# Kernel tuning notes

Hardware: AMD Instinct MI355X
Metric: run time of the kernel (lower is better)

## Reference

```python
import jax, jax.numpy as jnp
import numpy as np

B, T, C = 4, 2048, 1024
N_HEAD = 16
HEAD_DIM = C // N_HEAD


def setup_inputs() -> dict:
    key = jax.random.key(0)
    k1, k2, k3 = jax.random.split(key, 3)
    x = jax.random.normal(k1, (B, T, C), dtype=jnp.float32)
    # Linear weights stored as (in, out); scaled like typical init
    w_qkv = jax.random.normal(k2, (C, 3 * C), dtype=jnp.float32) * (1.0 / np.sqrt(C))
    w_proj = jax.random.normal(k3, (C, C), dtype=jnp.float32) * (1.0 / np.sqrt(C))
    return {"x": x, "w_qkv": w_qkv, "w_proj": w_proj}


def reference(x, w_qkv, w_proj):
    b, t, c = x.shape
    qkv = x @ w_qkv                      # (B,T,3C)
    q, k, v = jnp.split(qkv, 3, axis=-1)
    # (B,H,T,D)
    def to_heads(a):
        return a.reshape(b, t, N_HEAD, HEAD_DIM).transpose(0, 2, 1, 3)
    q, k, v = to_heads(q), to_heads(k), to_heads(v)
    scale = 1.0 / np.sqrt(HEAD_DIM).astype(np.float32)
    att = jnp.einsum('bhqd,bhkd->bhqk', q, k) * scale   # (B,H,T,T)
    causal = jnp.tril(jnp.ones((t, t), dtype=bool))
    att = jnp.where(causal[None, None, :, :], att, -jnp.inf)
    att = jax.nn.softmax(att, axis=-1)
    # dropout p=0.0 (eval) -> identity
    y = jnp.einsum('bhqk,bhkd->bhqd', att, v)            # (B,H,T,D)
    y = y.transpose(0, 2, 1, 3).reshape(b, t, c)
    return y @ w_proj
```

## Files before the change

kernel.cpp:

```cpp
#include <hip/hip_runtime.h>
#include <hip/hip_bf16.h>
#include <stdint.h>

#define Bsz 4
#define Tsz 2048
#define Csz 1024
#define Hn  16
#define Dh  64
#define BH  (Bsz*Hn)
#define Mrows (Bsz*Tsz)
#define N1  (3*Csz)

typedef short s16x8 __attribute__((ext_vector_type(8)));
typedef short s16x4 __attribute__((ext_vector_type(4)));
typedef float fx4   __attribute__((ext_vector_type(4)));

static __device__ __forceinline__ short f2bf(float x) {
  __hip_bfloat16 h = __float2bfloat16(x);
  return __builtin_bit_cast(short, h);
}

#define GLDS16(g, l) __builtin_amdgcn_global_load_lds( \
    (const __attribute__((address_space(1))) void*)(g), \
    (__attribute__((address_space(3))) void*)(l), 16, 0, 0)

__global__ __launch_bounds__(256) void prep_kernel(
    const float* __restrict__ x,  short* __restrict__ xb,
    const float* __restrict__ wq, short* __restrict__ wqT,
    const float* __restrict__ wp, short* __restrict__ wpT)
{
  const int bid = (int)blockIdx.x;
  if (bid < 1024) {
    const int n4 = Mrows*Csz/4;
    int i = bid * 256 + threadIdx.x;
    const int stride = 1024 * 256;
    for (; i < n4; i += stride) {
      float4 v = ((const float4*)x)[i];
      s16x4 o;
      o.x = f2bf(v.x); o.y = f2bf(v.y); o.z = f2bf(v.z); o.w = f2bf(v.w);
      ((s16x4*)xb)[i] = o;
    }
    return;
  }
  const float* w; short* wt; int K, N, tb;
  if (bid < 1024 + 3072) { w = wq; wt = wqT; K = Csz; N = N1;  tb = bid - 1024; }
  else                   { w = wp; wt = wpT; K = Csz; N = Csz; tb = bid - 4096; }
  const int nbx = N >> 5;
  const int n0 = (tb % nbx) * 32;
  const int k0 = (tb / nbx) * 32;
  __shared__ float tile[32][33];
  int tc = threadIdx.x & 31;
  int tr = threadIdx.x >> 5;
#pragma unroll
  for (int p = 0; p < 4; p++) {
    int r = tr + p*8;
    tile[r][tc] = w[(size_t)(k0 + r) * N + (n0 + tc)];
  }
  __syncthreads();
#pragma unroll
  for (int p = 0; p < 4; p++) {
    int r = tr + p*8;
    wt[(size_t)(n0 + r) * K + (k0 + tc)] = f2bf(tile[tc][r]);
  }
}

static __device__ __forceinline__ s16x8 lds_frag(const short* p, int off) {
  return *(const s16x8*)(p + off);
}

#define WAITV(n) __asm__ __volatile__("s_waitcnt vmcnt(" #n ")" ::: "memory")

__global__ __launch_bounds__(512) void gemm_bt_kernel(
    const short* __restrict__ A, const short* __restrict__ Bt,
    float* __restrict__ Cf,
    short* __restrict__ Qo, short* __restrict__ Ko, short* __restrict__ Vo,
    int Mdim, int Ndim, int Kdim, int mode)
{
  __shared__ __align__(16) short sA[3][128*64];
  __shared__ __align__(16) short sB[3][256*64];
  const int tid  = threadIdx.x;
  const int lane = tid & 63;
  const int lr   = lane & 15;
  const int lq   = lane >> 4;
  const int wv   = tid >> 6;
  const int nb   = Ndim >> 8;
  const int nwg  = (int)gridDim.x;
  const int orig = (int)blockIdx.x;
  const int wgid = (orig & 7) * (nwg >> 3) + (orig >> 3);
  const int bm   = wgid / nb;
  const int bn   = wgid % nb;
  const int m_off = (wv & 1) << 6;
  const int n_off = (wv >> 1) << 6;

  const short* Ab = A  + (size_t)bm * 128 * Kdim;
  const short* Bb = Bt + (size_t)bn * 256 * Kdim;

  const short* gA[2];
  const short* gB[4];
#pragma unroll
  for (int j = 0; j < 2; j++) {
    int c = tid + 512*j, r = c >> 3, o = ((c & 7) ^ (r & 7)) * 8;
    gA[j] = Ab + (size_t)r * Kdim + o;
  }
#pragma unroll
  for (int j = 0; j < 4; j++) {
    int c = tid + 512*j, r = c >> 3, o = ((c & 7) ^ (r & 7)) * 8;
    gB[j] = Bb + (size_t)r * Kdim + o;
  }

  int offA[4][2], offB[4][2];
#pragma unroll
  for (int ft = 0; ft < 4; ft++)
#pragma unroll
    for (int kk = 0; kk < 2; kk++) {
      int ra = m_off + ft*16 + lr;
      offA[ft][kk] = ra*64 + ((((kk<<2) | lq) ^ (ra & 7)) << 3);
      int rb = n_off + ft*16 + lr;
      offB[ft][kk] = rb*64 + ((((kk<<2) | lq) ^ (rb & 7)) << 3);
    }

  fx4 acc[4][4];
#pragma unroll
  for (int i = 0; i < 4; i++)
#pragma unroll
    for (int j = 0; j < 4; j++) acc[i][j] = (fx4){0.f, 0.f, 0.f, 0.f};

  auto STAGE_P1 = [&](int k0, short* dA, short* dB) {
    GLDS16(gA[0] + k0, dA + tid*8);
    GLDS16(gA[1] + k0, dA + (tid+512)*8);
    GLDS16(gB[0] + k0, dB + tid*8);
  };
  auto STAGE_P2 = [&](int k0, short* dB) {
    GLDS16(gB[1] + k0, dB + (tid+512)*8);
    GLDS16(gB[2] + k0, dB + (tid+1024)*8);
    GLDS16(gB[3] + k0, dB + (tid+1536)*8);
  };

  const int NIT = Kdim >> 6;

  STAGE_P1(0,  sA[0], sB[0]); STAGE_P2(0,  sB[0]);
  STAGE_P1(64, sA[1], sB[1]); STAGE_P2(64, sB[1]);
  WAITV(6);
  __builtin_amdgcn_s_barrier();

  const short *cA = sA[0], *cB = sB[0];
  const short *nA = sA[1], *nB = sB[1];
  short *eA = sA[2], *eB = sB[2];

  for (int t = 0; t < NIT; ++t) {
    if (t + 2 < NIT) STAGE_P1((t+2)*64, eA, eB);

    s16x8 af[4][2], bf[2][2];
#pragma unroll
    for (int mt = 0; mt < 4; mt++)
#pragma unroll
      for (int kk = 0; kk < 2; kk++)
        af[mt][kk] = lds_frag(cA, offA[mt][kk]);
#pragma unroll
    for (int nt = 0; nt < 2; nt++)
#pragma unroll
      for (int kk = 0; kk < 2; kk++)
        bf[nt][kk] = lds_frag(cB, offB[nt][kk]);
    __builtin_amdgcn_s_setprio(1);
#pragma unroll
    for (int kk = 0; kk < 2; kk++)
#pragma unroll
      for (int mt = 0; mt < 4; mt++) {
        acc[mt][0] = __builtin_amdgcn_mfma_f32_16x16x32_bf16(af[mt][kk], bf[0][kk], acc[mt][0], 0, 0, 0);
        acc[mt][1] = __builtin_amdgcn_mfma_f32_16x16x32_bf16(af[mt][kk], bf[1][kk], acc[mt][1], 0, 0, 0);
      }
    __builtin_amdgcn_s_setprio(0);
    __builtin_amdgcn_sched_barrier(0);
    __builtin_amdgcn_s_barrier();

    if (t + 2 < NIT) STAGE_P2((t+2)*64, eB);
#pragma unroll
    for (int nt = 0; nt < 2; nt++)
#pragma unroll
      for (int kk = 0; kk < 2; kk++)
        bf[nt][kk] = lds_frag(cB, offB[nt+2][kk]);
    __builtin_amdgcn_s_setprio(1);
#pragma unroll
    for (int kk = 0; kk < 2; kk++)
#pragma unroll
      for (int mt = 0; mt < 4; mt++) {
        acc[mt][2] = __builtin_amdgcn_mfma_f32_16x16x32_bf16(af[mt][kk], bf[0][kk], acc[mt][2], 0, 0, 0);
        acc[mt][3] = __builtin_amdgcn_mfma_f32_16x16x32_bf16(af[mt][kk], bf[1][kk], acc[mt][3], 0, 0, 0);
      }
    __builtin_amdgcn_s_setprio(0);
    __builtin_amdgcn_sched_barrier(0);
    if (t + 2 < NIT)      { WAITV(6); }
    else if (t + 1 < NIT) { WAITV(0); }
    __builtin_amdgcn_s_barrier();

    const short *tAp = cA, *tBp = cB;
    cA = nA; cB = nB;
    nA = eA; nB = eB;
    eA = (short*)tAp; eB = (short*)tBp;
  }

  const int gm0 = bm*128 + m_off;
  const int gn0 = bn*256 + n_off;
  if (mode == 0) {
#pragma unroll
    for (int mt = 0; mt < 4; mt++)
#pragma unroll
      for (int nt = 0; nt < 4; nt++) {
        int col = gn0 + nt*16 + lr;
#pragma unroll
        for (int r = 0; r < 4; r++) {
          int row = gm0 + mt*16 + lq*4 + r;
          Cf[(size_t)row * Ndim + col] = acc[mt][nt][r];
        }
      }
  } else {
#pragma unroll
    for (int mt = 0; mt < 4; mt++)
#pragma unroll
      for (int nt = 0; nt < 4; nt++) {
        int n   = gn0 + nt*16 + lr;
        int sec = n >> 10;
        int cc  = n & 1023;
        int hh  = cc >> 6;
        int dd  = cc & 63;
        if (sec == 2) {
          int tt0 = gm0 + mt*16 + lq*4;
          int bb  = tt0 >> 11;
          int bh  = bb * Hn + hh;
          s16x4 pk;
          pk.x = f2bf(acc[mt][nt][0]); pk.y = f2bf(acc[mt][nt][1]);
          pk.z = f2bf(acc[mt][nt][2]); pk.w = f2bf(acc[mt][nt][3]);
          *(s16x4*)(Vo + ((size_t)bh * Dh + dd) * Tsz + (tt0 & 2047)) = pk;
        } else {
#pragma unroll
          for (int r = 0; r < 4; r++) {
            int m  = gm0 + mt*16 + lq*4 + r;
            int bb = m >> 11;
            int tt = m & 2047;
            int bh = bb * Hn + hh;
            short v = f2bf(acc[mt][nt][r]);
            if (sec == 0) Qo[((size_t)bh * Tsz + tt) * Dh + dd] = v;
            else          Ko[((size_t)bh * Tsz + tt) * Dh + dd] = v;
          }
        }
      }
  }
}

#define PPITCH 72

static __device__ __forceinline__ void attn_stage(
    const short* __restrict__ Kp, const short* __restrict__ Vp, int kbase,
    short* __restrict__ sK, short* __restrict__ sV,
    int c0, int r0, int g0, int c1, int r1, int g1)
{
  GLDS16(Kp + (size_t)(kbase + r0)*Dh + g0, sK + c0*8);
  GLDS16(Kp + (size_t)(kbase + r1)*Dh + g1, sK + c1*8);
  GLDS16(Vp + (size_t)r0*Tsz + kbase + g0, sV + c0*8);
  GLDS16(Vp + (size_t)r1*Tsz + kbase + g1, sV + c1*8);
}

static __device__ __forceinline__ void attn_compute(
    const short* __restrict__ sK, const short* __restrict__ sV,
    int kbase, int q0, int lr, int lq, int sw,
    short* __restrict__ pb, const s16x8 bq[2][2], fx4 o[2][4], float li[2])
{
  const float sc = 0.125f * 1.44269504f;
  const bool masked = (kbase + 63 > q0);

  fx4 s[2][4];
#pragma unroll
  for (int j = 0; j < 2; j++)
#pragma unroll
    for (int mt = 0; mt < 4; mt++) s[j][mt] = (fx4){0.f,0.f,0.f,0.f};
  __builtin_amdgcn_s_setprio(1);
#pragma unroll
  for (int mt = 0; mt < 4; mt++)
#pragma unroll
    for (int kk = 0; kk < 2; kk++) {
      const s16x8 akf = *(const s16x8*)(sK + (mt*16 + lr)*64 + ((kk*4 + lq) ^ sw)*8);
      s[0][mt] = __builtin_amdgcn_mfma_f32_16x16x32_bf16(akf, bq[0][kk], s[0][mt], 0, 0, 0);
      s[1][mt] = __builtin_amdgcn_mfma_f32_16x16x32_bf16(akf, bq[1][kk], s[1][mt], 0, 0, 0);
    }
  __builtin_amdgcn_s_setprio(0);

#pragma unroll
  for (int j = 0; j < 2; j++) {
    const int qg = q0 + 16*j + lr;
    float p[16];
#pragma unroll
    for (int mt = 0; mt < 4; mt++)
#pragma unroll
      for (int r = 0; r < 4; r++) {
        float v = s[j][mt][r];
        if (masked) {
          int jg = kbase + mt*16 + lq*4 + r;
          v = (jg <= qg) ? v : -1e30f;
        }
        p[mt*4 + r] = __builtin_amdgcn_exp2f(v * sc);
      }
    float s8[8];
#pragma unroll
    for (int i = 0; i < 8; i++) s8[i] = p[i] + p[i+8];
    float s4[4];
#pragma unroll
    for (int i = 0; i < 4; i++) s4[i] = s8[i] + s8[i+4];
    li[j] += (s4[0] + s4[2]) + (s4[1] + s4[3]);
#pragma unroll
    for (int mt = 0; mt < 4; mt++) {
      s16x4 pk;
      pk.x = f2bf(p[mt*4+0]); pk.y = f2bf(p[mt*4+1]);
      pk.z = f2bf(p[mt*4+2]); pk.w = f2bf(p[mt*4+3]);
      *(s16x4*)(pb + (16*j + lr)*PPITCH + mt*16 + lq*4) = pk;
    }
  }
  __asm__ __volatile__("" ::: "memory");
  s16x8 pf[2][2];
#pragma unroll
  for (int j = 0; j < 2; j++)
#pragma unroll
    for (int kk = 0; kk < 2; kk++)
      pf[j][kk] = *(const s16x8*)(pb + (16*j + lr)*PPITCH + kk*32 + lq*8);
  __asm__ __volatile__("" ::: "memory");

  __builtin_amdgcn_s_setprio(1);
#pragma unroll
  for (int dt = 0; dt < 4; dt++)
#pragma unroll
    for (int kk = 0; kk < 2; kk++) {
      const s16x8 avf = *(const s16x8*)(sV + (dt*16 + lr)*64 + ((kk*4 + lq) ^ sw)*8);
      o[0][dt] = __builtin_amdgcn_mfma_f32_16x16x32_bf16(avf, pf[0][kk], o[0][dt], 0, 0, 0);
      o[1][dt] = __builtin_amdgcn_mfma_f32_16x16x32_bf16(avf, pf[1][kk], o[1][dt], 0, 0, 0);
    }
  __builtin_amdgcn_s_setprio(0);
}

__global__ __launch_bounds__(256) void attn_kernel(
    const short* __restrict__ Qb, const short* __restrict__ Kb,
    const short* __restrict__ Vt, short* __restrict__ Y)
{
  __shared__ __align__(16) short sK[2][64*64];
  __shared__ __align__(16) short sV[2][64*64];
  __shared__ __align__(16) short pbuf[4][32*PPITCH];
  const int tid  = threadIdx.x;
  const int lane = tid & 63;
  const int wv   = tid >> 6;
  const int lr   = lane & 15;
  const int lq   = lane >> 4;
  const int sw   = lr & 7;
  const int bh   = blockIdx.x;
  const int qb   = 15 - (int)blockIdx.y;
  const int b    = bh >> 4;
  const int h    = bh & 15;
  const int q0   = qb*128 + wv*32;

  const short* Qp = Qb + (size_t)bh * Tsz * Dh;
  const short* Kp = Kb + (size_t)bh * Tsz * Dh;
  const short* Vp = Vt + (size_t)bh * Dh * Tsz;
  short* pb = pbuf[wv];

  const int c0 = tid,       r0 = c0 >> 3, g0 = (((c0 & 7) ^ (r0 & 7)) * 8);
  const int c1 = tid + 256, r1 = c1 >> 3, g1 = (((c1 & 7) ^ (r1 & 7)) * 8);

  s16x8 bq[2][2];
#pragma unroll
  for (int j = 0; j < 2; j++)
#pragma unroll
    for (int kk = 0; kk < 2; kk++)
      bq[j][kk] = *(const s16x8*)(Qp + (size_t)(q0 + 16*j + lr)*Dh + kk*32 + lq*8);

  fx4 o[2][4];
#pragma unroll
  for (int j = 0; j < 2; j++)
#pragma unroll
    for (int i = 0; i < 4; i++) o[j][i] = (fx4){0.f, 0.f, 0.f, 0.f};
  float li[2] = {0.f, 0.f};

  const int ntiles = 2*qb + 2;
  attn_stage(Kp, Vp, 0, sK[0], sV[0], c0, r0, g0, c1, r1, g1);
  for (int kt = 0; kt < ntiles; kt += 2) {
    __syncthreads();
    if (kt + 1 < ntiles) attn_stage(Kp, Vp, (kt+1)*64, sK[1], sV[1], c0, r0, g0, c1, r1, g1);
    if (kt*64 <= q0 + 31)
      attn_compute(sK[0], sV[0], kt*64, q0, lr, lq, sw, pb, bq, o, li);
    __syncthreads();
    if (kt + 2 < ntiles) attn_stage(Kp, Vp, (kt+2)*64, sK[0], sV[0], c0, r0, g0, c1, r1, g1);
    if ((kt+1)*64 <= q0 + 31)
      attn_compute(sK[1], sV[1], (kt+1)*64, q0, lr, lq, sw, pb, bq, o, li);
  }

#pragma unroll
  for (int j = 0; j < 2; j++) {
    float l = li[j];
    l += __shfl_xor(l, 16);
    l += __shfl_xor(l, 32);
    float inv = 1.0f / l;
#pragma unroll
    for (int dt = 0; dt < 4; dt++) {
      s16x4 yk;
      yk.x = f2bf(o[j][dt][0]*inv); yk.y = f2bf(o[j][dt][1]*inv);
      yk.z = f2bf(o[j][dt][2]*inv); yk.w = f2bf(o[j][dt][3]*inv);
      *(s16x4*)(Y + ((size_t)b*Tsz + q0 + 16*j + lr)*Csz + h*Dh + dt*16 + lq*4) = yk;
    }
  }
}

extern "C" void kernel_launch(void* const* d_in, const int* in_sizes, int n_in,
                              void* d_out, int out_size, void* d_ws, size_t ws_size,
                              hipStream_t stream)
{
  const float* x  = (const float*)d_in[0];
  const float* wq = (const float*)d_in[1];
  const float* wp = (const float*)d_in[2];
  float* out = (float*)d_out;

  char* ws = (char*)d_ws;
  size_t off = 0;
  short* xb  = (short*)(ws + off); off += (size_t)Mrows*Csz*2;
  short* wqT = (short*)(ws + off); off += (size_t)N1*Csz*2;
  short* wpT = (short*)(ws + off); off += (size_t)Csz*Csz*2;
  short* Qb  = (short*)(ws + off); off += (size_t)BH*Tsz*Dh*2;
  short* Kb  = (short*)(ws + off); off += (size_t)BH*Tsz*Dh*2;
  short* Vt  = (short*)(ws + off); off += (size_t)BH*Dh*Tsz*2;
  short* Yb  = (short*)(ws + off); off += (size_t)Mrows*Csz*2;

  prep_kernel<<<1024 + 3072 + 1024, 256, 0, stream>>>(x, xb, wq, wqT, wp, wpT);
  gemm_bt_kernel<<<(Mrows/128)*(N1/256), 512, 0, stream>>>(
      xb, wqT, nullptr, Qb, Kb, Vt, Mrows, N1, Csz, 1);
  attn_kernel<<<dim3(BH, Tsz/128), 256, 0, stream>>>(Qb, Kb, Vt, Yb);
  gemm_bt_kernel<<<(Mrows/128)*(Csz/256), 512, 0, stream>>>(
      Yb, wpT, out, nullptr, nullptr, nullptr, Mrows, Csz, Csz, 0);
}
```

Measured before the change: 246.5 us.

## Add dedicated 256x256-tile QKV GEMM with double-buffered split-stage pipeline

Introduces a separate QKV projection kernel that uses 256x256 output tiles per workgroup (8 waves, each computing 128x64) with XOR-swizzled LDS and a two-buffer, finely interleaved load/compute schedule. The previous kernel used 128x256 tiles with triple buffering. The larger tiles raise arithmetic intensity and reuse of loaded A/B data. In exchange the grid is halved to 384 workgroups, which may underfill the GPU's CUs, and register pressure rises with 32 accumulators per wave. The output projection GEMM keeps the old kernel with its mode switch removed.

```diff
diff --git a/kernel.cpp b/kernel.cpp
--- a/kernel.cpp
+++ b/kernel.cpp
@@ -23,6 +23,11 @@
 #define GLDS16(g, l) __builtin_amdgcn_global_load_lds( \
     (const __attribute__((address_space(1))) void*)(g), \
     (__attribute__((address_space(3))) void*)(l), 16, 0, 0)
+
+#define WAITV(n) __asm__ __volatile__("s_waitcnt vmcnt(" #n ")" ::: "memory")
+#define LGKM0    __asm__ __volatile__("s_waitcnt lgkmcnt(0)" ::: "memory")
+#define SCHEDB   __builtin_amdgcn_sched_barrier(0)
+#define BAR      __builtin_amdgcn_s_barrier()
 
 __global__ __launch_bounds__(256) void prep_kernel(
     const float* __restrict__ x,  short* __restrict__ xb,
@@ -68,13 +73,265 @@
   return *(const s16x8*)(p + off);
 }
 
-#define WAITV(n) __asm__ __volatile__("s_waitcnt vmcnt(" #n ")" ::: "memory")
+__global__ __launch_bounds__(512) void gemm_qkv_kernel(
+    const short* __restrict__ A, const short* __restrict__ Bt,
+    short* __restrict__ Qo, short* __restrict__ Ko, short* __restrict__ Vo,
+    int Ndim, int Kdim)
+{
+  __shared__ __align__(16) short sA[2*16384];
+  __shared__ __align__(16) short sB[2*16384];
+  const int tid  = threadIdx.x;
+  const int lane = tid & 63;
+  const int lr   = lane & 15;
+  const int lq   = lane >> 4;
+  const int wv   = tid >> 6;
+  const int wm   = wv >> 2;
+  const int wn   = wv & 3;
+  const int nb   = Ndim >> 8;
+  const int nwg  = (int)gridDim.x;
+  const int orig = (int)blockIdx.x;
+  const int wgid = (orig & 7) * (nwg >> 3) + (orig >> 3);
+  const int bm   = wgid / nb;
+  const int bn   = wgid % nb;
+
+  const short* Ab = A  + (size_t)bm * 256 * Kdim;
+  const short* Bb = Bt + (size_t)bn * 256 * Kdim;
+
+  const short* gAs[2];
+  const short* gBs[2];
+  int ldso[2];
+#pragma unroll
+  for (int j = 0; j < 2; j++) {
+    int c = tid + 512*j, r = c >> 3, sl = ((c & 7) ^ (r & 7)) * 8;
+    gAs[j] = Ab + (size_t)r * Kdim + sl;
+    gBs[j] = Bb + (size_t)r * Kdim + sl;
+    ldso[j] = c * 8;
+  }
+
+  auto SA = [&](int t, int h) {
+#pragma unroll
+    for (int j = 0; j < 2; j++)
+      GLDS16(gAs[j] + (size_t)(h*128)*Kdim + t*64, sA + (t&1)*16384 + h*8192 + ldso[j]);
+  };
+  auto SB = [&](int t, int h) {
+#pragma unroll
+    for (int j = 0; j < 2; j++)
+      GLDS16(gBs[j] + (size_t)(h*128)*Kdim + t*64, sB + (t&1)*16384 + h*8192 + ldso[j]);
+  };
+
+  int offA[8][2], offB[4][2];
+#pragma unroll
+  for (int mt = 0; mt < 8; mt++)
+#pragma unroll
+    for (int kk = 0; kk < 2; kk++) {
+      int row = wm*128 + mt*16 + lr;
+      offA[mt][kk] = row*64 + ((((kk<<2)|lq) ^ (row & 7)) << 3);
+    }
+#pragma unroll
+  for (int nt = 0; nt < 4; nt++)
+#pragma unroll
+    for (int kk = 0; kk < 2; kk++) {
+      int row = wn*64 + nt*16 + lr;
+      offB[nt][kk] = row*64 + ((((kk<<2)|lq) ^ (row & 7)) << 3);
+    }
+
+  fx4 acc[8][4];
+#pragma unroll
+  for (int i = 0; i < 8; i++)
+#pragma unroll
+    for (int j = 0; j < 4; j++) acc[i][j] = (fx4){0.f, 0.f, 0.f, 0.f};
+
+  const int NT = Kdim >> 6;
+
+  SA(0,0); SA(0,1); SB(0,0); SB(0,1);
+  SB(1,0); SA(1,0);
+  WAITV(4);
+  BAR; SCHEDB;
+
+  for (int i = 0; i < NT/2; ++i) {
+    const int T1 = 2*i+1, Tp = 2*i+2, Tq = 2*i+3;
+    const short* bA0 = sA;            const short* bB0 = sB;
+    const short* bA1 = sA + 16384;    const short* bB1 = sB + 16384;
+    s16x8 afr[4][2], bf0[2][2], bf1[2][2];
+
+#pragma unroll
+    for (int m = 0; m < 4; m++)
+#pragma unroll
+      for (int k = 0; k < 2; k++) afr[m][k] = lds_frag(bA0, offA[m][k]);
+#pragma unroll
+    for (int n = 0; n < 2; n++)
+#pragma unroll
+      for (int k = 0; k < 2; k++) bf0[n][k] = lds_frag(bB0, offB[n][k]);
+    SB(T1, 1);
+    BAR; LGKM0; SCHEDB;
+    __builtin_amdgcn_s_setprio(1);
+#pragma unroll
+    for (int k = 0; k < 2; k++)
+#pragma unroll
+      for (int m = 0; m < 4; m++) {
+        acc[m][0] = __builtin_amdgcn_mfma_f32_16x16x32_bf16(afr[m][k], bf0[0][k], acc[m][0], 0, 0, 0);
+        acc[m][1] = __builtin_amdgcn_mfma_f32_16x16x32_bf16(afr[m][k], bf0[1][k], acc[m][1], 0, 0, 0);
+      }
+    __builtin_amdgcn_s_setprio(0);
+    SCHEDB; BAR;
+
+#pragma unroll
+    for (int n = 0; n < 2; n++)
+#pragma unroll
+      for (int k = 0; k < 2; k++) bf1[n][k] = lds_frag(bB0, offB[n+2][k]);
+    SA(T1, 1);
+    BAR; LGKM0; SCHEDB;
+    __builtin_amdgcn_s_setprio(1);
+#pragma unroll
+    for (int k = 0; k < 2; k++)
+#pragma unroll
+      for (int m = 0; m < 4; m++) {
+        acc[m][2] = __builtin_amdgcn_mfma_f32_16x16x32_bf16(afr[m][k], bf1[0][k], acc[m][2], 0, 0, 0);
+        acc[m][3] = __builtin_amdgcn_mfma_f32_16x16x32_bf16(afr[m][k], bf1[1][k], acc[m][3], 0, 0, 0);
+      }
+    __builtin_amdgcn_s_setprio(0);
+    SCHEDB; BAR;
+
+#pragma unroll
+    for (int m = 0; m < 4; m++)
+#pragma unroll
+      for (int k = 0; k < 2; k++) afr[m][k] = lds_frag(bA0, offA[m+4][k]);
+    if (Tp < NT) SB(Tp, 0);
+    BAR; LGKM0; SCHEDB;
+    __builtin_amdgcn_s_setprio(1);
+#pragma unroll
+    for (int k = 0; k < 2; k++)
+#pragma unroll
+      for (int m = 0; m < 4; m++) {
+        acc[m+4][2] = __builtin_amdgcn_mfma_f32_16x16x32_bf16(afr[m][k], bf1[0][k], acc[m+4][2], 0, 0, 0);
+        acc[m+4][3] = __builtin_amdgcn_mfma_f32_16x16x32_bf16(afr[m][k], bf1[1][k], acc[m+4][3], 0, 0, 0);
+      }
+    __builtin_amdgcn_s_setprio(0);
+    SCHEDB; BAR;
+
+    if (Tp < NT) SB(Tp, 1);
+    BAR; SCHEDB;
+    __builtin_amdgcn_s_setprio(1);
+#pragma unroll
+    for (int k = 0; k < 2; k++)
+#pragma unroll
+      for (int m = 0; m < 4; m++) {
+        acc[m+4][0] = __builtin_amdgcn_mfma_f32_16x16x32_bf16(afr[m][k], bf0[0][k], acc[m+4][0], 0, 0, 0);
+        acc[m+4][1] = __builtin_amdgcn_mfma_f32_16x16x32_bf16(afr[m][k], bf0[1][k], acc[m+4][1], 0, 0, 0);
+      }
+    __builtin_amdgcn_s_setprio(0);
+    SCHEDB;
+    if (Tp < NT) { WAITV(4); } else { WAITV(0); }
+    BAR; SCHEDB;
+
+#pragma unroll
+    for (int m = 0; m < 4; m++)
+#pragma unroll
+      for (int k = 0; k < 2; k++) afr[m][k] = lds_frag(bA1, offA[m][k]);
+#pragma unroll
+    for (int n = 0; n < 2; n++)
+#pragma unroll
+      for (int k = 0; k < 2; k++) bf0[n][k] = lds_frag(bB1, offB[n][k]);
+    if (Tp < NT) SA(Tp, 0);
+    BAR; LGKM0; SCHEDB;
+    __builtin_amdgcn_s_setprio(1);
+#pragma unroll
+    for (int k = 0; k < 2; k++)
+#pragma unroll
+      for (int m = 0; m < 4; m++) {
+        acc[m][0] = __builtin_amdgcn_mfma_f32_16x16x32_bf16(afr[m][k], bf0[0][k], acc[m][0], 0, 0, 0);
+        acc[m][1] = __builtin_amdgcn_mfma_f32_16x16x32_bf16(afr[m][k], bf0[1][k], acc[m][1], 0, 0, 0);
+      }
+    __builtin_amdgcn_s_setprio(0);
+    SCHEDB; BAR;
+
+#pragma unroll
+    for (int n = 0; n < 2; n++)
+#pragma unroll
+      for (int k = 0; k < 2; k++) bf1[n][k] = lds_frag(bB1, offB[n+2][k]);
+    if (Tp < NT) SA(Tp, 1);
+    BAR; LGKM0; SCHEDB;
+    __builtin_amdgcn_s_setprio(1);
+#pragma unroll
+    for (int k = 0; k < 2; k++)
+#pragma unroll
+      for (int m = 0; m < 4; m++) {
+        acc[m][2] = __builtin_amdgcn_mfma_f32_16x16x32_bf16(afr[m][k], bf1[0][k], acc[m][2], 0, 0, 0);
+        acc[m][3] = __builtin_amdgcn_mfma_f32_16x16x32_bf16(afr[m][k], bf1[1][k], acc[m][3], 0, 0, 0);
+      }
+    __builtin_amdgcn_s_setprio(0);
+    SCHEDB; BAR;
+
+#pragma unroll
+    for (int m = 0; m < 4; m++)
+#pragma unroll
+      for (int k = 0; k < 2; k++) afr[m][k] = lds_frag(bA1, offA[m+4][k]);
+    if (Tq < NT) SB(Tq, 0);
+    BAR; LGKM0; SCHEDB;
+    __builtin_amdgcn_s_setprio(1);
+#pragma unroll
+    for (int k = 0; k < 2; k++)
+#pragma unroll
+      for (int m = 0; m < 4; m++) {
+        acc[m+4][2] = __builtin_amdgcn_mfma_f32_16x16x32_bf16(afr[m][k], bf1[0][k], acc[m+4][2], 0, 0, 0);
+        acc[m+4][3] = __builtin_amdgcn_mfma_f32_16x16x32_bf16(afr[m][k], bf1[1][k], acc[m+4][3], 0, 0, 0);
+      }
+    __builtin_amdgcn_s_setprio(0);
+    SCHEDB; BAR;
+
+    if (Tq < NT) SA(Tq, 0);
+    BAR; SCHEDB;
+    __builtin_amdgcn_s_setprio(1);
+#pragma unroll
+    for (int k = 0; k < 2; k++)
+#pragma unroll
+      for (int m = 0; m < 4; m++) {
+        acc[m+4][0] = __builtin_amdgcn_mfma_f32_16x16x32_bf16(afr[m][k], bf0[0][k], acc[m+4][0], 0, 0, 0);
+        acc[m+4][1] = __builtin_amdgcn_mfma_f32_16x16x32_bf16(afr[m][k], bf0[1][k], acc[m+4][1], 0, 0, 0);
+      }
+    __builtin_amdgcn_s_setprio(0);
+    SCHEDB;
+    if (Tq < NT) { WAITV(4); }
+    BAR; SCHEDB;
+  }
+
+  const int gm0 = bm*256 + wm*128;
+  const int gn0 = bn*256 + wn*64;
+#pragma unroll
+  for (int mt = 0; mt < 8; mt++)
+#pragma unroll
+    for (int nt = 0; nt < 4; nt++) {
+      int n   = gn0 + nt*16 + lr;
+      int sec = n >> 10;
+      int cc  = n & 1023;
+      int hh  = cc >> 6;
+      int dd  = cc & 63;
+      if (sec == 2) {
+        int tt0 = gm0 + mt*16 + lq*4;
+        int bb  = tt0 >> 11;
+        int bh  = bb * Hn + hh;
+        s16x4 pk;
+        pk.x = f2bf(acc[mt][nt][0]); pk.y = f2bf(acc[mt][nt][1]);
+        pk.z = f2bf(acc[mt][nt][2]); pk.w = f2bf(acc[mt][nt][3]);
+        *(s16x4*)(Vo + ((size_t)bh * Dh + dd) * Tsz + (tt0 & 2047)) = pk;
+      } else {
+#pragma unroll
+        for (int r = 0; r < 4; r++) {
+          int m  = gm0 + mt*16 + lq*4 + r;
+          int bb = m >> 11;
+          int tt = m & 2047;
+          int bh = bb * Hn + hh;
+          short v = f2bf(acc[mt][nt][r]);
+          if (sec == 0) Qo[((size_t)bh * Tsz + tt) * Dh + dd] = v;
+          else          Ko[((size_t)bh * Tsz + tt) * Dh + dd] = v;
+        }
+      }
+    }
+}
 
 __global__ __launch_bounds__(512) void gemm_bt_kernel(
     const short* __restrict__ A, const short* __restrict__ Bt,
-    float* __restrict__ Cf,
-    short* __restrict__ Qo, short* __restrict__ Ko, short* __restrict__ Vo,
-    int Mdim, int Ndim, int Kdim, int mode)
+    float* __restrict__ Cf, int Mdim, int Ndim, int Kdim)
 {
   __shared__ __align__(16) short sA[3][128*64];
   __shared__ __align__(16) short sB[3][256*64];
@@ -141,7 +398,7 @@
   STAGE_P1(0,  sA[0], sB[0]); STAGE_P2(0,  sB[0]);
   STAGE_P1(64, sA[1], sB[1]); STAGE_P2(64, sB[1]);
   WAITV(6);
-  __builtin_amdgcn_s_barrier();
+  BAR;
 
   const short *cA = sA[0], *cB = sB[0];
   const short *nA = sA[1], *nB = sB[1];
@@ -170,8 +427,8 @@
         acc[mt][1] = __builtin_amdgcn_mfma_f32_16x16x32_bf16(af[mt][kk], bf[1][kk], acc[mt][1], 0, 0, 0);
       }
     __builtin_amdgcn_s_setprio(0);
-    __builtin_amdgcn_sched_barrier(0);
-    __builtin_amdgcn_s_barrier();
+    SCHEDB;
+    BAR;
 
     if (t + 2 < NIT) STAGE_P2((t+2)*64, eB);
 #pragma unroll
@@ -188,10 +445,10 @@
         acc[mt][3] = __builtin_amdgcn_mfma_f32_16x16x32_bf16(af[mt][kk], bf[1][kk], acc[mt][3], 0, 0, 0);
       }
     __builtin_amdgcn_s_setprio(0);
-    __builtin_amdgcn_sched_barrier(0);
+    SCHEDB;
     if (t + 2 < NIT)      { WAITV(6); }
     else if (t + 1 < NIT) { WAITV(0); }
-    __builtin_amdgcn_s_barrier();
+    BAR;
 
     const short *tAp = cA, *tBp = cB;
     cA = nA; cB = nB;
@@ -201,50 +458,17 @@
 
   const int gm0 = bm*128 + m_off;
   const int gn0 = bn*256 + n_off;
-  if (mode == 0) {
-#pragma unroll
-    for (int mt = 0; mt < 4; mt++)
-#pragma unroll
-      for (int nt = 0; nt < 4; nt++) {
-        int col = gn0 + nt*16 + lr;
-#pragma unroll
-        for (int r = 0; r < 4; r++) {
-          int row = gm0 + mt*16 + lq*4 + r;
-          Cf[(size_t)row * Ndim + col] = acc[mt][nt][r];
-        }
-      }
-  } else {
-#pragma unroll
-    for (int mt = 0; mt < 4; mt++)
-#pragma unroll
-      for (int nt = 0; nt < 4; nt++) {
-        int n   = gn0 + nt*16 + lr;
-        int sec = n >> 10;
-        int cc  = n & 1023;
-        int hh  = cc >> 6;
-        int dd  = cc & 63;
-        if (sec == 2) {
-          int tt0 = gm0 + mt*16 + lq*4;
-          int bb  = tt0 >> 11;
-          int bh  = bb * Hn + hh;
-          s16x4 pk;
-          pk.x = f2bf(acc[mt][nt][0]); pk.y = f2bf(acc[mt][nt][1]);
-          pk.z = f2bf(acc[mt][nt][2]); pk.w = f2bf(acc[mt][nt][3]);
-          *(s16x4*)(Vo + ((size_t)bh * Dh + dd) * Tsz + (tt0 & 2047)) = pk;
-        } else {
-#pragma unroll
-          for (int r = 0; r < 4; r++) {
-            int m  = gm0 + mt*16 + lq*4 + r;
-            int bb = m >> 11;
-            int tt = m & 2047;
-            int bh = bb * Hn + hh;
-            short v = f2bf(acc[mt][nt][r]);
-            if (sec == 0) Qo[((size_t)bh * Tsz + tt) * Dh + dd] = v;
-            else          Ko[((size_t)bh * Tsz + tt) * Dh + dd] = v;
-          }
-        }
-      }
-  }
+#pragma unroll
+  for (int mt = 0; mt < 4; mt++)
+#pragma unroll
+    for (int nt = 0; nt < 4; nt++) {
+      int col = gn0 + nt*16 + lr;
+#pragma unroll
+      for (int r = 0; r < 4; r++) {
+        int row = gm0 + mt*16 + lq*4 + r;
+        Cf[(size_t)row * Ndim + col] = acc[mt][nt][r];
+      }
+    }
 }
 
 #define PPITCH 72
@@ -425,9 +649,9 @@
   short* Yb  = (short*)(ws + off); off += (size_t)Mrows*Csz*2;
 
   prep_kernel<<<1024 + 3072 + 1024, 256, 0, stream>>>(x, xb, wq, wqT, wp, wpT);
-  gemm_bt_kernel<<<(Mrows/128)*(N1/256), 512, 0, stream>>>(
-      xb, wqT, nullptr, Qb, Kb, Vt, Mrows, N1, Csz, 1);
+  gemm_qkv_kernel<<<(Mrows/256)*(N1/256), 512, 0, stream>>>(
+      xb, wqT, Qb, Kb, Vt, N1, Csz);
   attn_kernel<<<dim3(BH, Tsz/128), 256, 0, stream>>>(Qb, Kb, Vt, Yb);
   gemm_bt_kernel<<<(Mrows/128)*(Csz/256), 512, 0, stream>>>(
-      Yb, wpT, out, nullptr, nullptr, nullptr, Mrows, Csz, Csz, 0);
-}
+      Yb, wpT, out, Mrows, Csz, Csz);
+}
```

Measured after the change: 249.0 us. Within noise of the previous version (+1.0%).
